# Performance work log

Hardware: AMD Instinct MI355X
Metric: run time of the kernel (lower is better)

Reference implementation:

```python
import jax, jax.numpy as jnp
import numpy as np

VOXEL_SIZE = 0.4
PC_START = jnp.array([-75.2, -75.2], dtype=jnp.float32)
GAMMA = 1.1
RADII = (0.8, 1.6)
NSAMPLES = (16, 32)


def _sq_dist(a, b):
    # a:[N,3], b:[N,3] -> [N,N] squared distances (no [N,N,3] intermediate)
    sa = jnp.sum(a * a, axis=-1)
    sb = jnp.sum(b * b, axis=-1)
    return jnp.maximum(sa[:, None] + sb[None, :] - 2.0 * (a @ b.T), 0.0)


def _ball_group(d2, valid, pts, r, k):
    # CUDA ball_query semantics: first-k in-radius neighbor indices (index order),
    # empty slots padded with the first found index (0 if none).
    N = d2.shape[0]
    mask = (d2 < r * r) & valid[None, :]
    skey = jnp.where(mask, jnp.arange(N, dtype=jnp.int32)[None, :], N)
    idx = jnp.sort(skey, axis=-1)[:, :k]            # [N,k]
    first = idx[:, :1]
    idx = jnp.where(idx == N, first, idx)
    idx = jnp.where(idx == N, 0, idx)
    grouped_xyz = pts[idx, :3] - pts[:, None, :3]   # [N,k,3] relative xyz
    return jnp.concatenate([grouped_xyz, pts[idx, 3:5]], axis=-1)  # [N,k,5] (use_xyz)


def _mlp(x, ws, bs):
    for w, b in zip(ws, bs):
        x = jax.nn.relu(x @ w.T + b)
    return x


def _frame(pts, boxes, mlps, num_sample):
    # pts: [N,5] (x,y,z,intensity,time); boxes: [M,7]
    xy = pts[:, :2]
    coords = jnp.floor((xy - PC_START) / VOXEL_SIZE)              # per-point voxel xy coord
    qcoords = jnp.floor((boxes[:, :2] - PC_START) / VOXEL_SIZE)   # box voxel coords
    half_diag = jnp.linalg.norm(boxes[:, 3:5] * 0.5, axis=-1)
    rad_vox = jnp.ceil(half_diag * GAMMA / VOXEL_SIZE)
    dvox = jnp.abs(qcoords[:, None, :] - coords[None, :, :])      # [M,N,2]
    valid = jnp.any(jnp.all(dvox < rad_vox[:, None, None], axis=-1), axis=0)  # [N]

    # cylindrical_pool: per-box top-k points inside cylinder radius
    cur_radiis = half_diag * GAMMA
    dis = jnp.linalg.norm(boxes[:, None, :2] - xy[None, :, :], axis=-1)  # [M,N]
    point_mask = (dis <= cur_radiis[:, None]) & valid[None, :]
    sampled_mask, sampled_idx = jax.lax.top_k(point_mask.astype(pts.dtype), num_sample)

    # PointNet++ SA-MSG evaluated at every point (equivalent to unique->gather in torch src)
    d2 = _sq_dist(pts[:, :3], pts[:, :3])
    feats = [pts[:, :3]]  # use_absolute_xyz: concat query xyz first
    for r, k, (ws, bs) in zip(RADII, NSAMPLES, mlps):
        g = _ball_group(d2, valid, pts, r, k)
        feats.append(jnp.max(_mlp(g, ws, bs), axis=1))  # max-pool over neighbors
    feats = jnp.concatenate(feats, axis=-1)             # [N, 3+32+64]

    sampled_points = pts[sampled_idx] * sampled_mask[..., None]  # zero out-of-radius slots
    return sampled_points, feats[sampled_idx]


def _forward(points, trajectory_rois, params, num_sample):
    B, T, N, C = points.shape
    M = trajectory_rois.shape[2]
    sp, pf = jax.vmap(lambda p, b: _frame(p, b, params, num_sample))(
        points.reshape(B * T, N, C), trajectory_rois.reshape(B * T, M, -1))

    def _merge(x):
        x = x.reshape(B, T, M, num_sample, x.shape[-1])
        return x.transpose(0, 2, 1, 3, 4).reshape(B, M, T * num_sample, x.shape[-1])

    return _merge(sp), _merge(pf)


def setup_inputs():
    key = jax.random.key(0)
    ks = jax.random.split(key, 24)
    B, T, N, M = 2, 4, 4096, 128
    xy = jax.random.uniform(ks[0], (B, T, N, 2), minval=-74.0, maxval=74.0)
    z = jax.random.uniform(ks[1], (B, T, N, 1), minval=-2.0, maxval=4.0)
    inten = jax.random.uniform(ks[2], (B, T, N, 1))
    ts = jnp.broadcast_to(jnp.arange(T, dtype=jnp.float32)[None, :, None, None] * 0.1, (B, T, N, 1))
    points = jnp.concatenate([xy, z, inten, ts], axis=-1)
    bxy = jax.random.uniform(ks[3], (B, T, M, 2), minval=-70.0, maxval=70.0)
    bz = jax.random.uniform(ks[4], (B, T, M, 1), minval=-1.0, maxval=1.0)
    bdxy = jax.random.uniform(ks[5], (B, T, M, 2), minval=1.5, maxval=5.0)
    bdz = jax.random.uniform(ks[6], (B, T, M, 1), minval=1.0, maxval=2.0)
    bh = jax.random.uniform(ks[7], (B, T, M, 1), minval=0.0, maxval=6.28)
    trajectory_rois = jnp.concatenate([bxy, bz, bdxy, bdz, bh], axis=-1)
    inp = {"points": points, "trajectory_rois": trajectory_rois}
    dims = [("w00", 16, 5), ("w01", 16, 16), ("w02", 32, 16),
            ("w10", 32, 5), ("w11", 32, 32), ("w12", 64, 32)]
    for i, (nm, o, ic) in enumerate(dims):
        inp[nm] = jax.random.normal(ks[8 + i], (o, ic), dtype=jnp.float32) / np.sqrt(ic)
        inp["b" + nm[1:]] = jnp.zeros((o,), dtype=jnp.float32)
    inp["num_sample"] = 32
    return inp


def reference(points, trajectory_rois, w00, b00, w01, b01, w02, b02,
              w10, b10, w11, b11, w12, b12, num_sample):
    params = (((w00, w01, w02), (b00, b01, b02)),
              ((w10, w11, w12), (b10, b11, b12)))
    return _forward(points, trajectory_rois, params, num_sample)
```

## Files before the change

### kernel.cpp

```cpp
#include <hip/hip_runtime.h>
#include <hip/hip_bf16.h>
#include <stdint.h>

#define NFRM 8
#define NPTS 4096
#define NBOX 128
#define NS   32
#define TT   4
#define BB   2
#define FEATC 99
#define OUT1OFF (BB*NBOX*TT*NS*5)

#define WS_SPK    0u
#define WS_EPK    524288u
#define WS_FEATS  786432u
#define WS_SIDX   13762560u
#define WS_FLAGS  13893632u
#define WS_NCNT   14024704u
#define WS_NLST   14024736u
#define WS_VPK    14155808u
#define WS_VEK    14680096u
#define WS_VORIG  14942240u
#define WS_VCNT   15073312u
#define WS_WT     15073344u
#define WS_CCNT   15089728u

__global__ void k_prep(const float* __restrict__ pts, const float* __restrict__ rois,
                       float4* __restrict__ spk, float2* __restrict__ epk,
                       const float* __restrict__ w00,const float* __restrict__ w01,
                       const float* __restrict__ w02,const float* __restrict__ w10,
                       const float* __restrict__ w11,const float* __restrict__ w12,
                       float* __restrict__ wt, int* __restrict__ flags,
                       int* __restrict__ gcnt, int* __restrict__ ccnt)
{
    if (blockIdx.x == 128){
        int t = threadIdx.x;
        if (t == 0) *gcnt = 0;
        for (int idx=t; idx<80;   idx+=256){ int o=idx/5,  i=idx%5;  wt[      i*16+o]=w00[idx]; }
        for (int idx=t; idx<256;  idx+=256){ int o=idx/16, i=idx%16; wt[  80+ i*16+o]=w01[idx]; }
        for (int idx=t; idx<512;  idx+=256){ int o=idx/16, i=idx%16; wt[ 336+ i*32+o]=w02[idx]; }
        for (int idx=t; idx<160;  idx+=256){ int o=idx/5,  i=idx%5;  wt[ 848+ i*32+o]=w10[idx]; }
        for (int idx=t; idx<1024; idx+=256){ int o=idx/32, i=idx%32; wt[1008+ i*32+o]=w11[idx]; }
        for (int idx=t; idx<2048; idx+=256){ int o=idx/32, i=idx%32; wt[2032+ i*64+o]=w12[idx]; }
        return;
    }
    int f = blockIdx.x >> 4;
    int chunk = blockIdx.x & 15;
    int tid = threadIdx.x, wv = tid >> 6, lane = tid & 63;
    int n = (chunk << 8) | tid;
    __shared__ float bqx[NBOX], bqy[NBOX], brv[NBOX];
    __shared__ int wcnt[4];
    if (tid < NBOX){
        const float* bp = rois + (size_t)(f*NBOX + tid)*7;
        float bx=bp[0], by=bp[1], dx=bp[3], dy=bp[4];
        float hx=__fmul_rn(dx,0.5f), hy=__fmul_rn(dy,0.5f);
        float hd=sqrtf(__fadd_rn(__fmul_rn(hx,hx),__fmul_rn(hy,hy)));
        brv[tid]=ceilf(__fdiv_rn(__fmul_rn(hd,1.1f),0.4f));
        bqx[tid]=floorf(__fdiv_rn(__fsub_rn(bx,-75.2f),0.4f));
        bqy[tid]=floorf(__fdiv_rn(__fsub_rn(by,-75.2f),0.4f));
    }
    flags[f*NPTS+n] = 0;
    __syncthreads();
    const float* pp = pts + (size_t)(f*NPTS+n)*5;
    float x=pp[0], y=pp[1], z=pp[2], it=pp[3], ts=pp[4];
    float cx=floorf(__fdiv_rn(__fsub_rn(x,-75.2f),0.4f));
    float cy=floorf(__fdiv_rn(__fsub_rn(y,-75.2f),0.4f));
    bool pred=false;
    for (int m=0;m<NBOX;m++)
        if (fabsf(bqx[m]-cx)<brv[m] && fabsf(bqy[m]-cy)<brv[m]){ pred=true; break; }
    spk[f*NPTS+n]=make_float4(x,y,z,pred?1.f:0.f);
    epk[f*NPTS+n]=make_float2(it,ts);
    uint64_t m = __ballot(pred);
    if (lane == 0) wcnt[wv] = __popcll(m);
    __syncthreads();
    if (tid == 0) ccnt[f*16+chunk] = wcnt[0]+wcnt[1]+wcnt[2]+wcnt[3];
}

__global__ void k_valid(const float4* __restrict__ spk, const float2* __restrict__ epk,
                        const int* __restrict__ ccnt,
                        float4* __restrict__ vpk, float2* __restrict__ vek,
                        int* __restrict__ vorig, int* __restrict__ vcnt)
{
    int f = blockIdx.x >> 4;
    int chunk = blockIdx.x & 15;
    int tid = threadIdx.x, wv = tid >> 6, lane = tid & 63;
    __shared__ int wcnt[4];
    int base = 0;
    for (int i=0;i<chunk;i++) base += ccnt[f*16+i];
    int j = (chunk << 8) | tid;
    float4 q = spk[f*NPTS+j];
    float2 e = epk[f*NPTS+j];
    bool pred = q.w > 0.5f;
    uint64_t m = __ballot(pred);
    uint64_t below = (1ull<<lane)-1ull;
    int lp = __popcll(m & below);
    if (lane == 0) wcnt[wv] = __popcll(m);
    __syncthreads();
    int off = base;
    for (int w=0; w<wv; w++) off += wcnt[w];
    if (pred){
        int pos = off + lp;
        float sb = __fadd_rn(__fadd_rn(__fmul_rn(q.x,q.x),__fmul_rn(q.y,q.y)),__fmul_rn(q.z,q.z));
        vpk[f*NPTS+pos] = make_float4(q.x,q.y,q.z,sb);
        vek[f*NPTS+pos] = e;
        vorig[f*NPTS+pos] = j;
    }
    if (chunk == 15 && tid == 0){
        int t = base + wcnt[0]+wcnt[1]+wcnt[2]+wcnt[3];
        vcnt[f] = t;
    }
}

__global__ __launch_bounds__(256) void k_select(
    const float4* __restrict__ spk, const float2* __restrict__ epk,
    const float4* __restrict__ vpk, const int* __restrict__ vorig,
    const int* __restrict__ vcnt,
    const float* __restrict__ rois, float* __restrict__ out,
    int* __restrict__ sidx, int* __restrict__ flags,
    int* __restrict__ gcnt, int* __restrict__ glist)
{
    int wv = threadIdx.x >> 6, lane = threadIdx.x & 63;
    int id = blockIdx.x*4 + wv;
    int f = id >> 7, m = id & 127;
    const float* bp = rois + (size_t)(f*NBOX+m)*7;
    float bx=bp[0], by=bp[1], dx=bp[3], dy=bp[4];
    float hx=__fmul_rn(dx,0.5f), hy=__fmul_rn(dy,0.5f);
    float hd=sqrtf(__fadd_rn(__fmul_rn(hx,hx),__fmul_rn(hy,hy)));
    float rr=__fmul_rn(hd,1.1f);

    __shared__ int lt[4][32], lf[4][32];
    int* ltw = lt[wv];
    int* lfw = lf[wv];
    const float4* fsp = spk + f*NPTS;
    const float4* fvp = vpk + f*NPTS;
    const int*    fvo = vorig + f*NPTS;
    int vc = vcnt[f];
    uint64_t below = (1ull<<lane)-1ull;

    int cT=0;
    for (int v0=0; v0<vc; v0+=128){
        int viA = v0 + lane;
        int viB = v0 + 64 + lane;
        int vicA = min(viA, vc-1);
        int vicB = min(viB, vc-1);
        float4 qA = fvp[vicA];
        float4 qB = fvp[vicB];
        {
            float ddx=__fsub_rn(bx,qA.x), ddy=__fsub_rn(by,qA.y);
            float dis=sqrtf(__fadd_rn(__fmul_rn(ddx,ddx),__fmul_rn(ddy,ddy)));
            bool pm = (viA < vc) && (dis <= rr);
            uint64_t mT=__ballot(pm);
            if (pm){ int pos=cT+__popcll(mT&below); if (pos<32) ltw[pos]=fvo[vicA]; }
            cT += __popcll(mT);
            if (cT>=32) break;
        }
        if (v0 + 64 < vc){
            float ddx=__fsub_rn(bx,qB.x), ddy=__fsub_rn(by,qB.y);
            float dis=sqrtf(__fadd_rn(__fmul_rn(ddx,ddx),__fmul_rn(ddy,ddy)));
            bool pm = (viB < vc) && (dis <= rr);
            uint64_t mT=__ballot(pm);
            if (pm){ int pos=cT+__popcll(mT&below); if (pos<32) ltw[pos]=fvo[vicB]; }
            cT += __popcll(mT);
            if (cT>=32) break;
        }
    }
    int cF=0;
    for (int j0=0; j0<NPTS; j0+=64){
        int j=j0+lane;
        float4 q = fsp[j];
        float ddx=__fsub_rn(bx,q.x), ddy=__fsub_rn(by,q.y);
        float dis=sqrtf(__fadd_rn(__fmul_rn(ddx,ddx),__fmul_rn(ddy,ddy)));
        bool fl = !((dis <= rr) && (q.w > 0.5f));
        uint64_t mF=__ballot(fl);
        if (fl){ int pos=cF+__popcll(mF&below); if (pos<32) lfw[pos]=j; }
        cF += __popcll(mF);
        if (cF>=32) break;
    }
    cT = min(cT,32);
    if (lane < 32){
        int s = lane;
        bool masked = s < cT;
        int idx = masked ? ltw[s] : lfw[s-cT];
        float mk = masked ? 1.f : 0.f;
        sidx[(f*NBOX+m)*NS+s]=idx;
        int b = f >> 2, t = f & 3;
        size_t row = (((size_t)(b*NBOX+m))*TT + t)*NS + s;
        float4 q = fsp[idx]; float2 e = epk[f*NPTS+idx];
        float* o0 = out + row*5;
        o0[0]=q.x*mk; o0[1]=q.y*mk; o0[2]=q.z*mk; o0[3]=e.x*mk; o0[4]=e.y*mk;
        int old = atomicExch(&flags[f*NPTS+idx], 1);
        bool fresh = (old == 0);
        uint64_t mm = __ballot(fresh);
        if (fresh){
            int ldr = __ffsll((unsigned long long)mm) - 1;
            int base = 0;
            if (lane == ldr) base = atomicAdd(gcnt, __popcll(mm));
            base = __shfl(base, ldr);
            glist[base + __popcll(mm & below)] = (f<<12) | idx;
        }
    }
}

__global__ __launch_bounds__(256) void k_mlp(
    const float4* __restrict__ spk, const float2* __restrict__ epk,
    const float4* __restrict__ vpk, const float2* __restrict__ vek,
    const int* __restrict__ vcnt,
    const int* __restrict__ gcntp, const int* __restrict__ glist,
    float* __restrict__ feats, const float* __restrict__ wt,
    const float* __restrict__ b00,const float* __restrict__ b01,
    const float* __restrict__ b02,const float* __restrict__ b10,
    const float* __restrict__ b11,const float* __restrict__ b12)
{
    int gcnt = *gcntp;
    if ((int)blockIdx.x * 4 >= gcnt) return;
    int tid = threadIdx.x;
    int wv = tid >> 6, lane = tid & 63;
    __shared__ int lists[4][48];
    __shared__ float h1buf[4][8][36];
    __shared__ float h2buf[4][8][36];
    int* l1 = lists[wv];
    int* l2 = lists[wv]+16;
    float (*h1b)[36] = h1buf[wv];
    float (*h2b)[36] = h2buf[wv];

    float wr00[5], wr01[16], wr02[16], wr10[5], wr11[32], wr12[32];
    float br00=0.f, br01=0.f, br02=0.f, br10=0.f, br11=0.f, br12=0.f;
    #pragma unroll
    for (int i=0;i<5;i++){ wr00[i]=0.f; wr10[i]=0.f; }
    #pragma unroll
    for (int i=0;i<16;i++){ wr01[i]=0.f; wr02[i]=0.f; }
    #pragma unroll
    for (int i=0;i<32;i++){ wr11[i]=0.f; wr12[i]=0.f; }
    if (lane < 16){
        #pragma unroll
        for (int i=0;i<5;i++)  wr00[i]=wt[i*16+lane];
        br00=b00[lane];
        #pragma unroll
        for (int i=0;i<16;i++) wr01[i]=wt[80+i*16+lane];
        br01=b01[lane];
    }
    if (lane < 32){
        #pragma unroll
        for (int i=0;i<16;i++) wr02[i]=wt[336+i*32+lane];
        br02=b02[lane];
        #pragma unroll
        for (int i=0;i<5;i++)  wr10[i]=wt[848+i*32+lane];
        br10=b10[lane];
        #pragma unroll
        for (int i=0;i<32;i++) wr11[i]=wt[1008+i*32+lane];
        br11=b11[lane];
    }
    #pragma unroll
    for (int i=0;i<32;i++) wr12[i]=wt[2032+i*64+lane];
    br12=b12[lane];

    const float RR1 = (float)(0.8*0.8);
    const float RR2 = (float)(1.6*1.6);
    uint64_t below = (1ull<<lane)-1ull;

    for (int li = blockIdx.x*4 + wv; li < gcnt; li += 8192){
        int pe = glist[li];
        int f = pe >> 12, n = pe & 4095;
        const float4* fsp = spk + f*NPTS;
        const float2* fep = epk + f*NPTS;
        const float4* fvp = vpk + f*NPTS;
        const float2* fve = vek + f*NPTS;
        int vc = vcnt[f];
        float4 me = fsp[n];
        float sa = __fadd_rn(__fadd_rn(__fmul_rn(me.x,me.x),__fmul_rn(me.y,me.y)),__fmul_rn(me.z,me.z));

        int cnt1=0, cnt2=0;
        for (int v0=0; v0<vc; v0+=64){
            int vi = v0 + lane;
            int vic = min(vi, vc-1);
            float4 q = fvp[vic];
            float dot = __fadd_rn(__fadd_rn(__fmul_rn(me.x,q.x),__fmul_rn(me.y,q.y)),__fmul_rn(me.z,q.z));
            float d2 = fmaxf(__fsub_rn(__fadd_rn(sa,q.w),__fmul_rn(2.0f,dot)), 0.f);
            bool inb = (vi < vc);
            bool p1 = inb && (d2 < RR1);
            bool p2 = inb && (d2 < RR2);
            uint64_t m1 = __ballot(p1), m2 = __ballot(p2);
            if (p1){ int pos = cnt1 + __popcll(m1 & below); if (pos < 16) l1[pos] = vi; }
            if (p2){ int pos = cnt2 + __popcll(m2 & below); if (pos < 32) l2[pos] = vi; }
            cnt1 += __popcll(m1); cnt2 += __popcll(m2);
            if (cnt1 >= 16 && cnt2 >= 32) break;
        }
        cnt1 = min(cnt1,16); cnt2 = min(cnt2,32);

        float* fo = feats + (size_t)(f*NPTS+n)*FEATC;
        float4 q0 = fsp[0]; float2 e0 = fep[0];

        {
            float pmax = 0.f;
            #pragma unroll 1
            for (int kb=0; kb<16; kb+=8){
                float4 qb[8]; float2 eb[8];
                #pragma unroll
                for (int j=0;j<8;j++){
                    int kk = kb+j;
                    int vi = (cnt1>0) ? ((kk<cnt1)? l1[kk] : l1[0]) : -1;
                    if (vi >= 0){ qb[j]=fvp[vi]; eb[j]=fve[vi]; }
                    else        { qb[j]=q0;      eb[j]=e0; }
                }
                #pragma unroll
                for (int j=0;j<8;j++){
                    float a1 = br00;
                    a1 += __fsub_rn(qb[j].x,me.x)*wr00[0];
                    a1 += __fsub_rn(qb[j].y,me.y)*wr00[1];
                    a1 += __fsub_rn(qb[j].z,me.z)*wr00[2];
                    a1 += eb[j].x*wr00[3];
                    a1 += eb[j].y*wr00[4];
                    float h = fmaxf(a1,0.f);
                    if (lane < 16) h1b[j][lane] = h;
                }
                float a2[8] = {br01,br01,br01,br01,br01,br01,br01,br01};
                #pragma unroll
                for (int c4=0;c4<4;c4++){
                    float4 hv[8];
                    #pragma unroll
                    for (int j=0;j<8;j++) hv[j] = *(const float4*)&h1b[j][c4*4];
                    #pragma unroll
                    for (int cc=0;cc<4;cc++){
                        float w = wr01[c4*4+cc];
                        #pragma unroll
                        for (int j=0;j<8;j++){
                            float h = (cc==0)?hv[j].x:(cc==1)?hv[j].y:(cc==2)?hv[j].z:hv[j].w;
                            a2[j] += h*w;
                        }
                    }
                }
                #pragma unroll
                for (int j=0;j<8;j++){
                    float h = fmaxf(a2[j],0.f);
                    if (lane < 16) h2b[j][lane] = h;
                }
                float a3[8] = {br02,br02,br02,br02,br02,br02,br02,br02};
                #pragma unroll
                for (int c4=0;c4<4;c4++){
                    float4 hv[8];
                    #pragma unroll
                    for (int j=0;j<8;j++) hv[j] = *(const float4*)&h2b[j][c4*4];
                    #pragma unroll
                    for (int cc=0;cc<4;cc++){
                        float w = wr02[c4*4+cc];
                        #pragma unroll
                        for (int j=0;j<8;j++){
                            float h = (cc==0)?hv[j].x:(cc==1)?hv[j].y:(cc==2)?hv[j].z:hv[j].w;
                            a3[j] += h*w;
                        }
                    }
                }
                #pragma unroll
                for (int j=0;j<8;j++) pmax = fmaxf(pmax, fmaxf(a3[j],0.f));
            }
            if (lane < 3){
                float mv = (lane==0)? me.x : ((lane==1)? me.y : me.z);
                fo[lane] = mv;
            }
            if (lane < 32) fo[3+lane] = pmax;
        }

        {
            float pmax = 0.f;
            #pragma unroll 1
            for (int kb=0; kb<32; kb+=8){
                float4 qb[8]; float2 eb[8];
                #pragma unroll
                for (int j=0;j<8;j++){
                    int kk = kb+j;
                    int vi = (cnt2>0) ? ((kk<cnt2)? l2[kk] : l2[0]) : -1;
                    if (vi >= 0){ qb[j]=fvp[vi]; eb[j]=fve[vi]; }
                    else        { qb[j]=q0;      eb[j]=e0; }
                }
                #pragma unroll
                for (int j=0;j<8;j++){
                    float a1 = br10;
                    a1 += __fsub_rn(qb[j].x,me.x)*wr10[0];
                    a1 += __fsub_rn(qb[j].y,me.y)*wr10[1];
                    a1 += __fsub_rn(qb[j].z,me.z)*wr10[2];
                    a1 += eb[j].x*wr10[3];
                    a1 += eb[j].y*wr10[4];
                    float h = fmaxf(a1,0.f);
                    if (lane < 32) h1b[j][lane] = h;
                }
                float a2[8] = {br11,br11,br11,br11,br11,br11,br11,br11};
                #pragma unroll
                for (int c4=0;c4<8;c4++){
                    float4 hv[8];
                    #pragma unroll
                    for (int j=0;j<8;j++) hv[j] = *(const float4*)&h1b[j][c4*4];
                    #pragma unroll
                    for (int cc=0;cc<4;cc++){
                        float w = wr11[c4*4+cc];
                        #pragma unroll
                        for (int j=0;j<8;j++){
                            float h = (cc==0)?hv[j].x:(cc==1)?hv[j].y:(cc==2)?hv[j].z:hv[j].w;
                            a2[j] += h*w;
                        }
                    }
                }
                #pragma unroll
                for (int j=0;j<8;j++){
                    float h = fmaxf(a2[j],0.f);
                    if (lane < 32) h2b[j][lane] = h;
                }
                float a3[8] = {br12,br12,br12,br12,br12,br12,br12,br12};
                #pragma unroll
                for (int c4=0;c4<8;c4++){
                    float4 hv[8];
                    #pragma unroll
                    for (int j=0;j<8;j++) hv[j] = *(const float4*)&h2b[j][c4*4];
                    #pragma unroll
                    for (int cc=0;cc<4;cc++){
                        float w = wr12[c4*4+cc];
                        #pragma unroll
                        for (int j=0;j<8;j++){
                            float h = (cc==0)?hv[j].x:(cc==1)?hv[j].y:(cc==2)?hv[j].z:hv[j].w;
                            a3[j] += h*w;
                        }
                    }
                }
                #pragma unroll
                for (int j=0;j<8;j++) pmax = fmaxf(pmax, fmaxf(a3[j],0.f));
            }
            fo[35+lane] = pmax;
        }
    }
}

__global__ void k_gather(const float* __restrict__ feats, const int* __restrict__ sidx,
                         float* __restrict__ out)
{
    int id = blockIdx.x;
    int f = id >> 7, m = id & 127;
    int tid = threadIdx.x;
    int s = tid >> 3, j = tid & 7;
    int idx = sidx[(f*NBOX+m)*NS+s];
    int b = f >> 2, t = f & 3;
    size_t row = (((size_t)(b*NBOX+m))*TT + t)*NS + s;
    const float* fi = feats + (size_t)(f*NPTS+idx)*FEATC;
    float* o1 = out + OUT1OFF + row*FEATC;
    for (int c=j; c<FEATC; c+=8) o1[c]=fi[c];
}

extern "C" void kernel_launch(void* const* d_in, const int* in_sizes, int n_in,
                              void* d_out, int out_size, void* d_ws, size_t ws_size,
                              hipStream_t stream)
{
    const float* pts  = (const float*)d_in[0];
    const float* rois = (const float*)d_in[1];
    const float* w00=(const float*)d_in[2],  *b00=(const float*)d_in[3];
    const float* w01=(const float*)d_in[4],  *b01=(const float*)d_in[5];
    const float* w02=(const float*)d_in[6],  *b02=(const float*)d_in[7];
    const float* w10=(const float*)d_in[8],  *b10=(const float*)d_in[9];
    const float* w11=(const float*)d_in[10], *b11=(const float*)d_in[11];
    const float* w12=(const float*)d_in[12], *b12=(const float*)d_in[13];
    float* out = (float*)d_out;

    char* ws = (char*)d_ws;
    float4* spk   = (float4*)(ws + WS_SPK);
    float2* epk   = (float2*)(ws + WS_EPK);
    float*  feats = (float*) (ws + WS_FEATS);
    int*    sidx  = (int*)   (ws + WS_SIDX);
    int*    flags = (int*)   (ws + WS_FLAGS);
    int*    gcnt  = (int*)   (ws + WS_NCNT);
    int*    glist = (int*)   (ws + WS_NLST);
    float4* vpk   = (float4*)(ws + WS_VPK);
    float2* vek   = (float2*)(ws + WS_VEK);
    int*    vorig = (int*)   (ws + WS_VORIG);
    int*    vcnt  = (int*)   (ws + WS_VCNT);
    float*  wtr   = (float*) (ws + WS_WT);
    int*    ccnt  = (int*)   (ws + WS_CCNT);

    hipLaunchKernelGGL(k_prep,   dim3(NFRM*16+1), dim3(256), 0, stream,
                       pts, rois, spk, epk, w00,w01,w02,w10,w11,w12, wtr, flags, gcnt, ccnt);
    hipLaunchKernelGGL(k_valid,  dim3(NFRM*16), dim3(256), 0, stream,
                       spk, epk, ccnt, vpk, vek, vorig, vcnt);
    hipLaunchKernelGGL(k_select, dim3(NFRM*NBOX/4), dim3(256), 0, stream,
                       spk, epk, vpk, vorig, vcnt, rois, out, sidx, flags, gcnt, glist);
    hipLaunchKernelGGL(k_mlp,    dim3(2048), dim3(256), 0, stream,
                       spk, epk, vpk, vek, vcnt, gcnt, glist, feats, wtr,
                       b00,b01,b02,b10,b11,b12);
    hipLaunchKernelGGL(k_gather, dim3(NFRM*NBOX), dim3(256), 0, stream,
                       feats, sidx, out);
}
```

Before: 95.66 us.

## Pack multiple samples per wavefront to use idle lanes in narrow MLP layers

In the per-point MLP kernel, the narrow layers (16 and 32 channels) previously left 48 or 32 of 64 lanes idle. Lanes are now split into sub-groups that each process a different set of neighbor samples, so a 16-wide layer handles 4 sample groups and a 32-wide layer handles 2 at once. The shared buffers are enlarged to 16 rows, and partial maxima are combined with a cross-lane shuffle. This cuts idle-lane waste, at the cost of more shared memory and different loop trip counts.

```diff
diff --git a/kernel.cpp b/kernel.cpp
--- a/kernel.cpp
+++ b/kernel.cpp
@@ -215,41 +215,33 @@
     if ((int)blockIdx.x * 4 >= gcnt) return;
     int tid = threadIdx.x;
     int wv = tid >> 6, lane = tid & 63;
+    int g4 = lane >> 4, sl4 = lane & 15;
+    int g2 = lane >> 5, sl2 = lane & 31;
     __shared__ int lists[4][48];
-    __shared__ float h1buf[4][8][36];
-    __shared__ float h2buf[4][8][36];
+    __shared__ float h1buf[4][16][36];
+    __shared__ float h2buf[4][16][36];
     int* l1 = lists[wv];
     int* l2 = lists[wv]+16;
     float (*h1b)[36] = h1buf[wv];
     float (*h2b)[36] = h2buf[wv];
 
     float wr00[5], wr01[16], wr02[16], wr10[5], wr11[32], wr12[32];
-    float br00=0.f, br01=0.f, br02=0.f, br10=0.f, br11=0.f, br12=0.f;
-    #pragma unroll
-    for (int i=0;i<5;i++){ wr00[i]=0.f; wr10[i]=0.f; }
-    #pragma unroll
-    for (int i=0;i<16;i++){ wr01[i]=0.f; wr02[i]=0.f; }
-    #pragma unroll
-    for (int i=0;i<32;i++){ wr11[i]=0.f; wr12[i]=0.f; }
-    if (lane < 16){
-        #pragma unroll
-        for (int i=0;i<5;i++)  wr00[i]=wt[i*16+lane];
-        br00=b00[lane];
-        #pragma unroll
-        for (int i=0;i<16;i++) wr01[i]=wt[80+i*16+lane];
-        br01=b01[lane];
-    }
-    if (lane < 32){
-        #pragma unroll
-        for (int i=0;i<16;i++) wr02[i]=wt[336+i*32+lane];
-        br02=b02[lane];
-        #pragma unroll
-        for (int i=0;i<5;i++)  wr10[i]=wt[848+i*32+lane];
-        br10=b10[lane];
-        #pragma unroll
-        for (int i=0;i<32;i++) wr11[i]=wt[1008+i*32+lane];
-        br11=b11[lane];
-    }
+    float br00, br01, br02, br10, br11, br12;
+    #pragma unroll
+    for (int i=0;i<5;i++)  wr00[i]=wt[i*16+sl4];
+    br00=b00[sl4];
+    #pragma unroll
+    for (int i=0;i<16;i++) wr01[i]=wt[80+i*16+sl4];
+    br01=b01[sl4];
+    #pragma unroll
+    for (int i=0;i<16;i++) wr02[i]=wt[336+i*32+sl2];
+    br02=b02[sl2];
+    #pragma unroll
+    for (int i=0;i<5;i++)  wr10[i]=wt[848+i*32+sl2];
+    br10=b10[sl2];
+    #pragma unroll
+    for (int i=0;i<32;i++) wr11[i]=wt[1008+i*32+sl2];
+    br11=b11[sl2];
     #pragma unroll
     for (int i=0;i<32;i++) wr12[i]=wt[2032+i*64+lane];
     br12=b12[lane];
@@ -291,83 +283,77 @@
         float4 q0 = fsp[0]; float2 e0 = fep[0];
 
         {
-            float pmax = 0.f;
-            #pragma unroll 1
-            for (int kb=0; kb<16; kb+=8){
-                float4 qb[8]; float2 eb[8];
-                #pragma unroll
-                for (int j=0;j<8;j++){
-                    int kk = kb+j;
-                    int vi = (cnt1>0) ? ((kk<cnt1)? l1[kk] : l1[0]) : -1;
-                    if (vi >= 0){ qb[j]=fvp[vi]; eb[j]=fve[vi]; }
-                    else        { qb[j]=q0;      eb[j]=e0; }
-                }
-                #pragma unroll
-                for (int j=0;j<8;j++){
-                    float a1 = br00;
-                    a1 += __fsub_rn(qb[j].x,me.x)*wr00[0];
-                    a1 += __fsub_rn(qb[j].y,me.y)*wr00[1];
-                    a1 += __fsub_rn(qb[j].z,me.z)*wr00[2];
-                    a1 += eb[j].x*wr00[3];
-                    a1 += eb[j].y*wr00[4];
-                    float h = fmaxf(a1,0.f);
-                    if (lane < 16) h1b[j][lane] = h;
-                }
-                float a2[8] = {br01,br01,br01,br01,br01,br01,br01,br01};
-                #pragma unroll
-                for (int c4=0;c4<4;c4++){
-                    float4 hv[8];
-                    #pragma unroll
-                    for (int j=0;j<8;j++) hv[j] = *(const float4*)&h1b[j][c4*4];
-                    #pragma unroll
-                    for (int cc=0;cc<4;cc++){
-                        float w = wr01[c4*4+cc];
-                        #pragma unroll
-                        for (int j=0;j<8;j++){
-                            float h = (cc==0)?hv[j].x:(cc==1)?hv[j].y:(cc==2)?hv[j].z:hv[j].w;
-                            a2[j] += h*w;
-                        }
+            float4 qb[4]; float2 eb[4];
+            #pragma unroll
+            for (int j=0;j<4;j++){
+                int kk = g4*4 + j;
+                int vi = (cnt1>0) ? ((kk<cnt1)? l1[kk] : l1[0]) : -1;
+                if (vi >= 0){ qb[j]=fvp[vi]; eb[j]=fve[vi]; }
+                else        { qb[j]=q0;      eb[j]=e0; }
+            }
+            #pragma unroll
+            for (int j=0;j<4;j++){
+                float a1 = br00;
+                a1 += __fsub_rn(qb[j].x,me.x)*wr00[0];
+                a1 += __fsub_rn(qb[j].y,me.y)*wr00[1];
+                a1 += __fsub_rn(qb[j].z,me.z)*wr00[2];
+                a1 += eb[j].x*wr00[3];
+                a1 += eb[j].y*wr00[4];
+                h1b[g4*4+j][sl4] = fmaxf(a1,0.f);
+            }
+            float a2[4] = {br01,br01,br01,br01};
+            #pragma unroll
+            for (int c4=0;c4<4;c4++){
+                float4 hv[4];
+                #pragma unroll
+                for (int j=0;j<4;j++) hv[j] = *(const float4*)&h1b[g4*4+j][c4*4];
+                #pragma unroll
+                for (int cc=0;cc<4;cc++){
+                    float w = wr01[c4*4+cc];
+                    #pragma unroll
+                    for (int j=0;j<4;j++){
+                        float h = (cc==0)?hv[j].x:(cc==1)?hv[j].y:(cc==2)?hv[j].z:hv[j].w;
+                        a2[j] += h*w;
                     }
                 }
-                #pragma unroll
-                for (int j=0;j<8;j++){
-                    float h = fmaxf(a2[j],0.f);
-                    if (lane < 16) h2b[j][lane] = h;
-                }
-                float a3[8] = {br02,br02,br02,br02,br02,br02,br02,br02};
-                #pragma unroll
-                for (int c4=0;c4<4;c4++){
-                    float4 hv[8];
-                    #pragma unroll
-                    for (int j=0;j<8;j++) hv[j] = *(const float4*)&h2b[j][c4*4];
-                    #pragma unroll
-                    for (int cc=0;cc<4;cc++){
-                        float w = wr02[c4*4+cc];
-                        #pragma unroll
-                        for (int j=0;j<8;j++){
-                            float h = (cc==0)?hv[j].x:(cc==1)?hv[j].y:(cc==2)?hv[j].z:hv[j].w;
-                            a3[j] += h*w;
-                        }
+            }
+            #pragma unroll
+            for (int j=0;j<4;j++) h2b[g4*4+j][sl4] = fmaxf(a2[j],0.f);
+            float a3[8] = {br02,br02,br02,br02,br02,br02,br02,br02};
+            #pragma unroll
+            for (int c4=0;c4<4;c4++){
+                float4 hv[8];
+                #pragma unroll
+                for (int jj=0;jj<8;jj++) hv[jj] = *(const float4*)&h2b[g2*8+jj][c4*4];
+                #pragma unroll
+                for (int cc=0;cc<4;cc++){
+                    float w = wr02[c4*4+cc];
+                    #pragma unroll
+                    for (int jj=0;jj<8;jj++){
+                        float h = (cc==0)?hv[jj].x:(cc==1)?hv[jj].y:(cc==2)?hv[jj].z:hv[jj].w;
+                        a3[jj] += h*w;
                     }
                 }
-                #pragma unroll
-                for (int j=0;j<8;j++) pmax = fmaxf(pmax, fmaxf(a3[j],0.f));
-            }
+            }
+            float pm0 = 0.f;
+            #pragma unroll
+            for (int jj=0;jj<8;jj++) pm0 = fmaxf(pm0, fmaxf(a3[jj],0.f));
+            pm0 = fmaxf(pm0, __shfl_xor(pm0, 32));
             if (lane < 3){
                 float mv = (lane==0)? me.x : ((lane==1)? me.y : me.z);
                 fo[lane] = mv;
             }
-            if (lane < 32) fo[3+lane] = pmax;
+            if (lane < 32) fo[3+lane] = pm0;
         }
 
         {
             float pmax = 0.f;
             #pragma unroll 1
-            for (int kb=0; kb<32; kb+=8){
+            for (int kb=0; kb<32; kb+=16){
                 float4 qb[8]; float2 eb[8];
                 #pragma unroll
                 for (int j=0;j<8;j++){
-                    int kk = kb+j;
+                    int kk = kb + g2*8 + j;
                     int vi = (cnt2>0) ? ((kk<cnt2)? l2[kk] : l2[0]) : -1;
                     if (vi >= 0){ qb[j]=fvp[vi]; eb[j]=fve[vi]; }
                     else        { qb[j]=q0;      eb[j]=e0; }
@@ -380,15 +366,14 @@
                     a1 += __fsub_rn(qb[j].z,me.z)*wr10[2];
                     a1 += eb[j].x*wr10[3];
                     a1 += eb[j].y*wr10[4];
-                    float h = fmaxf(a1,0.f);
-                    if (lane < 32) h1b[j][lane] = h;
+                    h1b[g2*8+j][sl2] = fmaxf(a1,0.f);
                 }
                 float a2[8] = {br11,br11,br11,br11,br11,br11,br11,br11};
                 #pragma unroll
                 for (int c4=0;c4<8;c4++){
                     float4 hv[8];
                     #pragma unroll
-                    for (int j=0;j<8;j++) hv[j] = *(const float4*)&h1b[j][c4*4];
+                    for (int j=0;j<8;j++) hv[j] = *(const float4*)&h1b[g2*8+j][c4*4];
                     #pragma unroll
                     for (int cc=0;cc<4;cc++){
                         float w = wr11[c4*4+cc];
@@ -400,28 +385,28 @@
                     }
                 }
                 #pragma unroll
-                for (int j=0;j<8;j++){
-                    float h = fmaxf(a2[j],0.f);
-                    if (lane < 32) h2b[j][lane] = h;
-                }
-                float a3[8] = {br12,br12,br12,br12,br12,br12,br12,br12};
-                #pragma unroll
-                for (int c4=0;c4<8;c4++){
-                    float4 hv[8];
-                    #pragma unroll
-                    for (int j=0;j<8;j++) hv[j] = *(const float4*)&h2b[j][c4*4];
-                    #pragma unroll
-                    for (int cc=0;cc<4;cc++){
-                        float w = wr12[c4*4+cc];
+                for (int j=0;j<8;j++) h2b[g2*8+j][sl2] = fmaxf(a2[j],0.f);
+                #pragma unroll 1
+                for (int half=0; half<2; half++){
+                    float a3[8] = {br12,br12,br12,br12,br12,br12,br12,br12};
+                    #pragma unroll
+                    for (int c4=0;c4<8;c4++){
+                        float4 hv[8];
                         #pragma unroll
-                        for (int j=0;j<8;j++){
-                            float h = (cc==0)?hv[j].x:(cc==1)?hv[j].y:(cc==2)?hv[j].z:hv[j].w;
-                            a3[j] += h*w;
+                        for (int jj=0;jj<8;jj++) hv[jj] = *(const float4*)&h2b[half*8+jj][c4*4];
+                        #pragma unroll
+                        for (int cc=0;cc<4;cc++){
+                            float w = wr12[c4*4+cc];
+                            #pragma unroll
+                            for (int jj=0;jj<8;jj++){
+                                float h = (cc==0)?hv[jj].x:(cc==1)?hv[jj].y:(cc==2)?hv[jj].z:hv[jj].w;
+                                a3[jj] += h*w;
+                            }
                         }
                     }
-                }
-                #pragma unroll
-                for (int j=0;j<8;j++) pmax = fmaxf(pmax, fmaxf(a3[j],0.f));
+                    #pragma unroll
+                    for (int jj=0;jj<8;jj++) pmax = fmaxf(pmax, fmaxf(a3[jj],0.f));
+                }
             }
             fo[35+lane] = pmax;
         }
```

Result: slower. 104.8 us (+9.6%).
